# Optimization experiments

Measured on AMD Instinct MI355X. Metric: run time of the kernel, lower is better.

The kernel has to match this reference:

```python
import jax, jax.numpy as jnp
import numpy as np
from jax import lax

T_STEPS = 16
TAU = 2.0
ALPHA = 4.0  # sigmoid surrogate sharpness
BN_EPS = 1e-5


def conv1d(x, w, b, stride, pad):
    # x: [N,C,L], w: [O,I,K]
    y = lax.conv_general_dilated(x, w, (stride,), [(pad, pad)],
                                 dimension_numbers=('NCH', 'OIH', 'NCH'))
    return y + b[None, :, None]


def maxpool1d(x):  # kernel 3, stride 2, pad 1 (pad value -inf via init)
    return lax.reduce_window(x, -jnp.inf, lax.max, (1, 1, 3), (1, 1, 2),
                             [(0, 0), (0, 0), (1, 1)])


def spike(x):  # heaviside forward (surrogate only matters for bwd)
    return (x >= 0).astype(x.dtype)


def lif(x_seq):
    # multi-step LIF: v += (x - v)/tau (v_reset=0), spike at v>=1, hard reset, detach_reset
    def step(v, x):
        v = v + (x - v) / TAU
        s = spike(v - 1.0)
        v = v * (1.0 - lax.stop_gradient(s))
        return v, s
    _, s_seq = lax.scan(step, jnp.zeros_like(x_seq[0]), x_seq)
    return s_seq


def seq_apply(f, xs):
    # apply stateless layer over [T,B,...] by folding T into batch
    T, B = xs.shape[0], xs.shape[1]
    y = f(xs.reshape((T * B,) + xs.shape[2:]))
    return y.reshape((T, B) + y.shape[1:])


def setup_inputs() -> dict:
    key = jax.random.key(0)
    ks = jax.random.split(key, 12)
    B, L = 256, 4097
    inp = {
        'x': jax.random.normal(ks[0], (B, L), jnp.float32),
        'conv0_w': jax.random.normal(ks[1], (16, 1, 7), jnp.float32) * 0.2,
        'conv0_b': jax.random.normal(ks[2], (16,), jnp.float32) * 0.1,
        'bn_g': jnp.ones((16,), jnp.float32),
        'bn_b': jnp.zeros((16,), jnp.float32),
        'bn_m': jax.random.normal(ks[3], (16,), jnp.float32) * 0.1,
        'bn_v': jnp.ones((16,), jnp.float32),
        'conv1_w': jax.random.normal(ks[4], (32, 16, 5), jnp.float32) * 0.1,
        'conv1_b': jax.random.normal(ks[5], (32,), jnp.float32) * 0.1,
        'conv2_w': jax.random.normal(ks[6], (64, 32, 3), jnp.float32) * 0.1,
        'conv2_b': jax.random.normal(ks[7], (64,), jnp.float32) * 0.1,
        'fc1_w': jax.random.normal(ks[8], (32, 64), jnp.float32) * 0.12,
        'fc1_b': jax.random.normal(ks[9], (32,), jnp.float32) * 0.1,
        'fc2_w': jax.random.normal(ks[10], (5, 32), jnp.float32) * 0.17,
        'fc2_b': jax.random.normal(ks[11], (5,), jnp.float32) * 0.1,
    }
    return inp


def reference(x, conv0_w, conv0_b, bn_g, bn_b, bn_m, bn_v,
              conv1_w, conv1_b, conv2_w, conv2_b,
              fc1_w, fc1_b, fc2_w, fc2_b):
    # ---- static encoder ----
    h = x[:, None, :]                                  # [B,1,4097]
    h = conv1d(h, conv0_w, conv0_b, 2, 3)              # [B,16,2049]
    h = (h - bn_m[None, :, None]) * lax.rsqrt(bn_v + BN_EPS)[None, :, None] \
        * bn_g[None, :, None] + bn_b[None, :, None]
    h = jax.nn.relu(h)
    h = maxpool1d(h)                                   # [B,16,1025]
    # ---- repeat over T timesteps ----
    hs = jnp.broadcast_to(h[None], (T_STEPS,) + h.shape)  # [T,B,16,1025]
    # ---- spiking trunk ----
    hs = seq_apply(lambda a: conv1d(a, conv1_w, conv1_b, 2, 2), hs)  # [T,B,32,513]
    hs = lif(hs)
    hs = seq_apply(maxpool1d, hs)                      # [T,B,32,257]
    hs = seq_apply(lambda a: conv1d(a, conv2_w, conv2_b, 2, 1), hs)  # [T,B,64,129]
    hs = lif(hs)
    # dropout: identity (inference); adaptive avg pool to 1 + flatten
    hs = hs.mean(axis=-1)                              # [T,B,64]
    # ---- classifier ----
    hs = jnp.einsum('tbd,od->tbo', hs, fc1_w) + fc1_b  # [T,B,32]
    hs = lif(hs)
    hs = jnp.einsum('tbd,od->tbo', hs, fc2_w) + fc2_b  # [T,B,5]
    return hs.mean(axis=0)                             # [B,5]
```

## Files before the change

kernel.cpp:

```cpp
#include <hip/hip_runtime.h>
#include <math.h>


#define NB 256
#define LX 4097
#define LQ 2049
#define LP 1025
#define LJ1 513
#define LP1 257
#define LJ2 129

#define M1S 520
#define S2R 132
#define HSW 260

typedef float f32x4 __attribute__((ext_vector_type(4)));

__global__ __launch_bounds__(256) void kF_front(const float* __restrict__ x,
                                                const float* __restrict__ w0,
                                                const float* __restrict__ b0,
                                                const float* __restrict__ bng,
                                                const float* __restrict__ bnb,
                                                const float* __restrict__ bnm,
                                                const float* __restrict__ bnv,
                                                const float* __restrict__ w1,
                                                const float* __restrict__ b1,
                                                unsigned short* __restrict__ m1,
                                                const float* __restrict__ w2,
                                                float* __restrict__ w2t) {
  __shared__ __align__(16) float xs[1052];
  __shared__ __align__(16) float hs[16 * HSW];
  __shared__ __align__(16) float wl[2560];
  __shared__ float w0s[112];
  __shared__ float cpar[64];
  __shared__ float rs_l[16];
  int bid = blockIdx.x;
  int b = bid / 5, jt = bid % 5;
  int J0 = jt * 128;
  int Pstart = 2 * J0 - 2;
  int tid = threadIdx.x;

  if (tid < 16) rs_l[tid] = (float)(1.0 / sqrt((double)bnv[tid] + 1e-5));
  {
    const float* xb = x + (size_t)b * LX;
    int xoff = 4 * Pstart - 5;
    for (int i = tid; i < 1052; i += 256) {
      int gi = xoff + i;
      xs[i] = (gi >= 0 && gi < LX) ? xb[gi] : 0.f;
    }
    for (int i = tid; i < 2560; i += 256) {
      int c = i & 31, r = i >> 5;
      wl[i] = w1[c * 80 + r];
    }
    if (tid < 112) w0s[tid] = w0[tid];
    if (tid >= 128 && tid < 192) {
      int i = tid - 128;
      int c = i >> 2, e = i & 3;
      float v = (e == 0) ? bnm[c] : (e == 1) ? bng[c] : (e == 2) ? bnb[c] : b0[c];
      cpar[i] = v;
    }
  }
  __syncthreads();

  for (int item = tid; item < 16 * 261; item += 256) {
    int c = item / 261, dp = item - c * 261;
    int p = Pstart + dp;
    float hm = 0.f;
    if (p >= 0 && p < LP) {
      const f32x4* xv = (const f32x4*)(xs + 4 * dp);
      f32x4 a = xv[0], bq = xv[1], cq = xv[2];
      float win[12] = {a.x, a.y, a.z, a.w, bq.x, bq.y, bq.z, bq.w,
                       cq.x, cq.y, cq.z, cq.w};
      float m = cpar[4 * c], g = cpar[4 * c + 1], bb = cpar[4 * c + 2],
            bc = cpar[4 * c + 3];
      float rs = rs_l[c];
      float wv[7];
#pragma unroll
      for (int k = 0; k < 7; ++k) wv[k] = w0s[c * 7 + k];
      float best = -INFINITY;
#pragma unroll
      for (int dq = -1; dq <= 1; ++dq) {
        int q = 2 * p + dq;
        if (q < 0 || q >= LQ) continue;
        float s = 0.f;
        int base = 2 * dq + 2;
#pragma unroll
        for (int k = 0; k < 7; ++k) s = fmaf(win[base + k], wv[k], s);
        float y = s + bc;
        y = (y - m) * rs * g + bb;
        y = fmaxf(y, 0.f);
        best = fmaxf(best, y);
      }
      hm = best;
    }
    hs[c * HSW + dp] = hm;
  }
  __syncthreads();

  {
    int c = tid & 31, jg = tid >> 5;
    int jbase = J0 + jg * 16;
    if (jbase <= 512) {
      float acc[16];
#pragma unroll
      for (int i = 0; i < 16; ++i) acc[i] = 0.f;

      for (int ic = 0; ic < 16; ++ic) {
        float win[36];
        const f32x4* row = (const f32x4*)(hs + ic * HSW + 32 * jg);
#pragma unroll
        for (int i = 0; i < 9; ++i) {
          f32x4 v = row[i];
          win[4 * i] = v.x; win[4 * i + 1] = v.y;
          win[4 * i + 2] = v.z; win[4 * i + 3] = v.w;
        }
        float wv[5];
#pragma unroll
        for (int k = 0; k < 5; ++k) wv[k] = wl[(ic * 5 + k) * 32 + c];
#pragma unroll
        for (int j = 0; j < 16; ++j) {
#pragma unroll
          for (int k = 0; k < 5; ++k) acc[j] = fmaf(win[2 * j + k], wv[k], acc[j]);
        }
      }

      float bc = b1[c];
      unsigned mskv[16];
#pragma unroll
      for (int j = 0; j < 16; ++j) {
        float xin = acc[j] + bc;
        float v = 0.f; unsigned mm = 0;
#pragma unroll
        for (int t = 0; t < 16; ++t) {
          v = v + (xin - v) * 0.5f;
          if (v >= 1.f) { mm |= (1u << t); v = 0.f; }
        }
        mskv[j] = mm;
      }
      size_t rowo = ((size_t)b * 32 + c) * M1S + jbase;
      if (jbase + 15 < LJ1) {
        uint4 u0, u1;
        u0.x = mskv[0] | (mskv[1] << 16);
        u0.y = mskv[2] | (mskv[3] << 16);
        u0.z = mskv[4] | (mskv[5] << 16);
        u0.w = mskv[6] | (mskv[7] << 16);
        u1.x = mskv[8] | (mskv[9] << 16);
        u1.y = mskv[10] | (mskv[11] << 16);
        u1.z = mskv[12] | (mskv[13] << 16);
        u1.w = mskv[14] | (mskv[15] << 16);
        *(uint4*)(m1 + rowo) = u0;
        *(uint4*)(m1 + rowo + 8) = u1;
      } else {
        for (int j = 0; j < 16; ++j)
          if (jbase + j < LJ1) m1[rowo + j] = (unsigned short)mskv[j];
      }
    }
  }

  if (bid < 16) {
    for (int idx = bid * 256 + tid; idx < 64 * 32 * 3; idx += 4096) {
      int k = idx % 3; int r = idx / 3; int c = r % 32; int oc = r / 32;
      w2t[(c * 3 + k) * 64 + oc] = w2[idx];
    }
  }
}

__global__ __launch_bounds__(256) void kD_conv2_lif(const unsigned short* __restrict__ m1,
                                                    const float* __restrict__ w2t_g,
                                                    const float* __restrict__ b2,
                                                    unsigned short* __restrict__ s2) {
  __shared__ __align__(16) float F[288 * 20];
  __shared__ unsigned mval[288];
  __shared__ unsigned short mbuf[32 * 20];
  int bid = blockIdx.x;
  int b = bid / 33, jt = bid % 33;
  int j0 = jt * 4;
  int tid = threadIdx.x;
  int w = tid >> 6;
  int lane = tid & 63;

  const unsigned short* m1b = m1 + (size_t)b * 32 * M1S;
  int qbase = 4 * j0 - 3;
  for (int i = tid; i < 1024; i += 256) {
    int c = i >> 5, u = i & 31;
    if (u < 20) {
      int q = qbase + u;
      mbuf[c * 20 + u] = (q >= 0 && q <= 512) ? m1b[(size_t)c * M1S + q] : (unsigned short)0;
    }
  }
  __syncthreads();

  for (int it = tid; it < 288; it += 256) {
    int c = it / 9, idx = it - c * 9;
    int p = 2 * j0 - 1 + idx;
    unsigned m = 0;
    if (p >= 0 && p < LP1) {
      const unsigned short* mr = mbuf + c * 20;
      int l0 = 2 * idx;
      m = (unsigned)mr[l0] | (unsigned)mr[l0 + 1] | (unsigned)mr[l0 + 2];
    }
    mval[it] = m;
    f32x4* Fr = (f32x4*)(F + it * 20);
    f32x4 f0, f1, f2, f3;
    f0.x = (float)(m & 1u);         f0.y = (float)((m >> 1) & 1u);
    f0.z = (float)((m >> 2) & 1u);  f0.w = (float)((m >> 3) & 1u);
    f1.x = (float)((m >> 4) & 1u);  f1.y = (float)((m >> 5) & 1u);
    f1.z = (float)((m >> 6) & 1u);  f1.w = (float)((m >> 7) & 1u);
    f2.x = (float)((m >> 8) & 1u);  f2.y = (float)((m >> 9) & 1u);
    f2.z = (float)((m >> 10) & 1u); f2.w = (float)((m >> 11) & 1u);
    f3.x = (float)((m >> 12) & 1u); f3.y = (float)((m >> 13) & 1u);
    f3.z = (float)((m >> 14) & 1u); f3.w = (float)((m >> 15) & 1u);
    Fr[0] = f0; Fr[1] = f1; Fr[2] = f2; Fr[3] = f3;
  }
  __syncthreads();

  unsigned bits;
  {
    bool nz = false;
    if (lane < 32) {
      int base9 = lane * 9 + 2 * w;
      nz = (mval[base9] | mval[base9 + 1] | mval[base9 + 2]) != 0u;
    }
    bits = (unsigned)__ballot(nz);
  }

  float acc[16];
#pragma unroll
  for (int t = 0; t < 16; ++t) acc[t] = 0.f;

  const float* wrow = w2t_g + lane;
  while (bits) {
    int c = __builtin_ctz(bits);
    bits &= bits - 1;
    int base9 = c * 9 + 2 * w;
    unsigned mv0 = mval[base9];
    unsigned mv1 = mval[base9 + 1];
    unsigned mv2 = mval[base9 + 2];
    const float* wr = wrow + c * 192;
    const float* Fb = F + base9 * 20;
    if (mv0) {
      float wv = wr[0];
      const f32x4* Fp = (const f32x4*)Fb;
      f32x4 fv[4];
      fv[0] = Fp[0]; fv[1] = Fp[1]; fv[2] = Fp[2]; fv[3] = Fp[3];
#pragma unroll
      for (int t = 0; t < 16; ++t) acc[t] = fmaf(wv, fv[t >> 2][t & 3], acc[t]);
    }
    if (mv1) {
      float wv = wr[64];
      const f32x4* Fp = (const f32x4*)(Fb + 20);
      f32x4 fv[4];
      fv[0] = Fp[0]; fv[1] = Fp[1]; fv[2] = Fp[2]; fv[3] = Fp[3];
#pragma unroll
      for (int t = 0; t < 16; ++t) acc[t] = fmaf(wv, fv[t >> 2][t & 3], acc[t]);
    }
    if (mv2) {
      float wv = wr[128];
      const f32x4* Fp = (const f32x4*)(Fb + 40);
      f32x4 fv[4];
      fv[0] = Fp[0]; fv[1] = Fp[1]; fv[2] = Fp[2]; fv[3] = Fp[3];
#pragma unroll
      for (int t = 0; t < 16; ++t) acc[t] = fmaf(wv, fv[t >> 2][t & 3], acc[t]);
    }
  }

  int j = j0 + w;
  if (j < LJ2) {
    float bc = b2[lane];
    float v = 0.f; unsigned mm = 0;
#pragma unroll
    for (int t = 0; t < 16; ++t) {
      float xin = acc[t] + bc;
      v = v + (xin - v) * 0.5f;
      if (v >= 1.f) { mm |= (1u << t); v = 0.f; }
    }
    s2[((size_t)b * S2R + j) * 64 + lane] = (unsigned short)mm;
  }
}

__global__ __launch_bounds__(256) void kE_head(const unsigned short* __restrict__ s2,
                                               const float* __restrict__ fc1w,
                                               const float* __restrict__ fc1b,
                                               const float* __restrict__ fc2w,
                                               const float* __restrict__ fc2b,
                                               float* __restrict__ out) {
  __shared__ float meanL[16][64];
  __shared__ unsigned s3m[32];
  int b = blockIdx.x;
  int tid = threadIdx.x;
  int oc = tid >> 2, part = tid & 3;

  int jstart = (part == 0) ? 0 : 33 + (part - 1) * 32;
  int jcount = (part == 0) ? 33 : 32;
  const unsigned short* base = s2 + (size_t)b * S2R * 64 + oc;
  int cnt[16];
#pragma unroll
  for (int t = 0; t < 16; ++t) cnt[t] = 0;
  for (int u = 0; u < jcount; ++u) {
    unsigned m = base[(size_t)(jstart + u) * 64];
#pragma unroll
    for (int t = 0; t < 16; ++t) cnt[t] += (int)((m >> t) & 1u);
  }
#pragma unroll
  for (int t = 0; t < 16; ++t) {
    cnt[t] += __shfl_xor(cnt[t], 1);
    cnt[t] += __shfl_xor(cnt[t], 2);
  }
  if (part == 0) {
#pragma unroll
    for (int t = 0; t < 16; ++t) meanL[t][oc] = (float)cnt[t] / 129.f;
  }
  __syncthreads();

  if (tid < 32) {
    int o = tid;
    const float* wrow = fc1w + o * 64;
    float bb = fc1b[o];
    float v = 0.f;
    unsigned msk = 0;
    for (int t = 0; t < 16; ++t) {
      float s = 0.f;
      for (int d = 0; d < 64; ++d) s = fmaf(meanL[t][d], wrow[d], s);
      float xin = s + bb;
      v = v + (xin - v) * 0.5f;
      if (v >= 1.f) { msk |= (1u << t); v = 0.f; }
    }
    s3m[o] = msk;
  }
  __syncthreads();

  if (tid < 5) {
    int q = tid;
    const float* wrow = fc2w + q * 32;
    float bb = fc2b[q];
    float accs = 0.f;
    for (int t = 0; t < 16; ++t) {
      float s = 0.f;
      for (int o = 0; o < 32; ++o) s += (((s3m[o] >> t) & 1u) ? wrow[o] : 0.f);
      accs += (s + bb);
    }
    out[b * 5 + q] = accs / 16.f;
  }
}

extern "C" void kernel_launch(void* const* d_in, const int* in_sizes, int n_in,
                              void* d_out, int out_size, void* d_ws, size_t ws_size,
                              hipStream_t stream) {
  const float* x   = (const float*)d_in[0];
  const float* w0  = (const float*)d_in[1];
  const float* b0  = (const float*)d_in[2];
  const float* bng = (const float*)d_in[3];
  const float* bnb = (const float*)d_in[4];
  const float* bnm = (const float*)d_in[5];
  const float* bnv = (const float*)d_in[6];
  const float* w1  = (const float*)d_in[7];
  const float* b1  = (const float*)d_in[8];
  const float* w2  = (const float*)d_in[9];
  const float* b2  = (const float*)d_in[10];
  const float* f1w = (const float*)d_in[11];
  const float* f1b = (const float*)d_in[12];
  const float* f2w = (const float*)d_in[13];
  const float* f2b = (const float*)d_in[14];
  float* out = (float*)d_out;

  char* ws = (char*)d_ws;
  size_t sz_m1 = (size_t)NB * 32 * M1S * 2;
  size_t sz_s2 = (size_t)NB * S2R * 64 * 2;
  size_t off_s2 = sz_m1;
  size_t off_w2 = off_s2 + sz_s2;
  if (ws_size < off_w2 + 6144 * 4) return;

  unsigned short* m1 = (unsigned short*)ws;
  unsigned short* s2 = (unsigned short*)(ws + off_s2);
  float* w2t = (float*)(ws + off_w2);

  kF_front<<<NB * 5, 256, 0, stream>>>(x, w0, b0, bng, bnb, bnm, bnv, w1, b1, m1, w2, w2t);
  kD_conv2_lif<<<NB * 33, 256, 0, stream>>>(m1, w2t, b2, s2);
  kE_head<<<NB, 256, 0, stream>>>(s2, f1w, f1b, f2w, f2b, out);
}
```

Before: 121.1 us.

## Halve front-kernel LDS via two-pass channel staging, pack conv2 weights, rework head reduction

The front kernel now computes the pooled encoder output in two halves of 8 channels, accumulating conv1 across both passes. This halves the shared-memory staging buffer so more blocks can be resident, at the cost of extra barriers. Conv2 weights are repacked so the three taps for each (channel, out-channel) pair load as one float4 instead of three scalar loads. The head kernel now gives each wavefront a slice of positions and reduces spike counts through shared memory instead of shuffles.

```diff
diff --git a/kernel.cpp b/kernel.cpp
--- a/kernel.cpp
+++ b/kernel.cpp
@@ -27,9 +27,9 @@
                                                 const float* __restrict__ b1,
                                                 unsigned short* __restrict__ m1,
                                                 const float* __restrict__ w2,
-                                                float* __restrict__ w2t) {
+                                                float* __restrict__ w2t2) {
   __shared__ __align__(16) float xs[1052];
-  __shared__ __align__(16) float hs[16 * HSW];
+  __shared__ __align__(16) float hs[8 * HSW];
   __shared__ __align__(16) float wl[2560];
   __shared__ float w0s[112];
   __shared__ float cpar[64];
@@ -62,52 +62,62 @@
   }
   __syncthreads();
 
-  for (int item = tid; item < 16 * 261; item += 256) {
-    int c = item / 261, dp = item - c * 261;
-    int p = Pstart + dp;
-    float hm = 0.f;
-    if (p >= 0 && p < LP) {
-      const f32x4* xv = (const f32x4*)(xs + 4 * dp);
-      f32x4 a = xv[0], bq = xv[1], cq = xv[2];
-      float win[12] = {a.x, a.y, a.z, a.w, bq.x, bq.y, bq.z, bq.w,
-                       cq.x, cq.y, cq.z, cq.w};
-      float m = cpar[4 * c], g = cpar[4 * c + 1], bb = cpar[4 * c + 2],
-            bc = cpar[4 * c + 3];
-      float rs = rs_l[c];
+  int c = tid & 31, jg = tid >> 5;
+  int jbase = J0 + jg * 16;
+  bool active = (jbase <= 512);
+  float acc[16];
+#pragma unroll
+  for (int i = 0; i < 16; ++i) acc[i] = 0.f;
+
+  for (int half = 0; half < 2; ++half) {
+    {
+      int c2l = tid >> 5;
+      int g2 = tid & 31;
+      int cc = half * 8 + c2l;
+      float m = cpar[4 * cc], g = cpar[4 * cc + 1], bb = cpar[4 * cc + 2],
+            bc = cpar[4 * cc + 3];
+      float rs = rs_l[cc];
       float wv[7];
 #pragma unroll
-      for (int k = 0; k < 7; ++k) wv[k] = w0s[c * 7 + k];
-      float best = -INFINITY;
-#pragma unroll
-      for (int dq = -1; dq <= 1; ++dq) {
-        int q = 2 * p + dq;
-        if (q < 0 || q >= LQ) continue;
-        float s = 0.f;
-        int base = 2 * dq + 2;
-#pragma unroll
-        for (int k = 0; k < 7; ++k) s = fmaf(win[base + k], wv[k], s);
-        float y = s + bc;
-        y = (y - m) * rs * g + bb;
-        y = fmaxf(y, 0.f);
-        best = fmaxf(best, y);
+      for (int k = 0; k < 7; ++k) wv[k] = w0s[cc * 7 + k];
+#pragma unroll
+      for (int i = 0; i < 9; ++i) {
+        int dp = g2 * 9 + i;
+        if (dp < 261) {
+          int p = Pstart + dp;
+          float hm = 0.f;
+          if (p >= 0 && p < LP) {
+            const f32x4* xv = (const f32x4*)(xs + 4 * dp);
+            f32x4 a = xv[0], bq = xv[1], cq = xv[2];
+            float win[12] = {a.x, a.y, a.z, a.w, bq.x, bq.y, bq.z, bq.w,
+                             cq.x, cq.y, cq.z, cq.w};
+            float best = -INFINITY;
+#pragma unroll
+            for (int dq = -1; dq <= 1; ++dq) {
+              int q = 2 * p + dq;
+              if (q < 0 || q >= LQ) continue;
+              float s = 0.f;
+              int base = 2 * dq + 2;
+#pragma unroll
+              for (int k = 0; k < 7; ++k) s = fmaf(win[base + k], wv[k], s);
+              float y = s + bc;
+              y = (y - m) * rs * g + bb;
+              y = fmaxf(y, 0.f);
+              best = fmaxf(best, y);
+            }
+            hm = best;
+          }
+          hs[c2l * HSW + dp] = hm;
+        }
       }
-      hm = best;
-    }
-    hs[c * HSW + dp] = hm;
-  }
-  __syncthreads();
-
-  {
-    int c = tid & 31, jg = tid >> 5;
-    int jbase = J0 + jg * 16;
-    if (jbase <= 512) {
-      float acc[16];
-#pragma unroll
-      for (int i = 0; i < 16; ++i) acc[i] = 0.f;
-
-      for (int ic = 0; ic < 16; ++ic) {
+    }
+    __syncthreads();
+
+    if (active) {
+      for (int icl = 0; icl < 8; ++icl) {
+        int ic = half * 8 + icl;
         float win[36];
-        const f32x4* row = (const f32x4*)(hs + ic * HSW + 32 * jg);
+        const f32x4* row = (const f32x4*)(hs + icl * HSW + 32 * jg);
 #pragma unroll
         for (int i = 0; i < 9; ++i) {
           f32x4 v = row[i];
@@ -123,50 +133,53 @@
           for (int k = 0; k < 5; ++k) acc[j] = fmaf(win[2 * j + k], wv[k], acc[j]);
         }
       }
-
-      float bc = b1[c];
-      unsigned mskv[16];
-#pragma unroll
-      for (int j = 0; j < 16; ++j) {
-        float xin = acc[j] + bc;
-        float v = 0.f; unsigned mm = 0;
-#pragma unroll
-        for (int t = 0; t < 16; ++t) {
-          v = v + (xin - v) * 0.5f;
-          if (v >= 1.f) { mm |= (1u << t); v = 0.f; }
-        }
-        mskv[j] = mm;
+    }
+    __syncthreads();
+  }
+
+  if (active) {
+    float bc = b1[c];
+    unsigned mskv[16];
+#pragma unroll
+    for (int j = 0; j < 16; ++j) {
+      float xin = acc[j] + bc;
+      float v = 0.f; unsigned mm = 0;
+#pragma unroll
+      for (int t = 0; t < 16; ++t) {
+        v = v + (xin - v) * 0.5f;
+        if (v >= 1.f) { mm |= (1u << t); v = 0.f; }
       }
-      size_t rowo = ((size_t)b * 32 + c) * M1S + jbase;
-      if (jbase + 15 < LJ1) {
-        uint4 u0, u1;
-        u0.x = mskv[0] | (mskv[1] << 16);
-        u0.y = mskv[2] | (mskv[3] << 16);
-        u0.z = mskv[4] | (mskv[5] << 16);
-        u0.w = mskv[6] | (mskv[7] << 16);
-        u1.x = mskv[8] | (mskv[9] << 16);
-        u1.y = mskv[10] | (mskv[11] << 16);
-        u1.z = mskv[12] | (mskv[13] << 16);
-        u1.w = mskv[14] | (mskv[15] << 16);
-        *(uint4*)(m1 + rowo) = u0;
-        *(uint4*)(m1 + rowo + 8) = u1;
-      } else {
-        for (int j = 0; j < 16; ++j)
-          if (jbase + j < LJ1) m1[rowo + j] = (unsigned short)mskv[j];
-      }
+      mskv[j] = mm;
+    }
+    size_t rowo = ((size_t)b * 32 + c) * M1S + jbase;
+    if (jbase + 15 < LJ1) {
+      uint4 u0, u1;
+      u0.x = mskv[0] | (mskv[1] << 16);
+      u0.y = mskv[2] | (mskv[3] << 16);
+      u0.z = mskv[4] | (mskv[5] << 16);
+      u0.w = mskv[6] | (mskv[7] << 16);
+      u1.x = mskv[8] | (mskv[9] << 16);
+      u1.y = mskv[10] | (mskv[11] << 16);
+      u1.z = mskv[12] | (mskv[13] << 16);
+      u1.w = mskv[14] | (mskv[15] << 16);
+      *(uint4*)(m1 + rowo) = u0;
+      *(uint4*)(m1 + rowo + 8) = u1;
+    } else {
+      for (int j = 0; j < 16; ++j)
+        if (jbase + j < LJ1) m1[rowo + j] = (unsigned short)mskv[j];
     }
   }
 
   if (bid < 16) {
     for (int idx = bid * 256 + tid; idx < 64 * 32 * 3; idx += 4096) {
-      int k = idx % 3; int r = idx / 3; int c = r % 32; int oc = r / 32;
-      w2t[(c * 3 + k) * 64 + oc] = w2[idx];
+      int k = idx % 3; int r = idx / 3; int cc = r % 32; int oc = r / 32;
+      w2t2[((size_t)cc * 64 + oc) * 4 + k] = w2[idx];
     }
   }
 }
 
 __global__ __launch_bounds__(256) void kD_conv2_lif(const unsigned short* __restrict__ m1,
-                                                    const float* __restrict__ w2t_g,
+                                                    const float* __restrict__ w2t2,
                                                     const float* __restrict__ b2,
                                                     unsigned short* __restrict__ s2) {
   __shared__ __align__(16) float F[288 * 20];
@@ -228,7 +241,7 @@
 #pragma unroll
   for (int t = 0; t < 16; ++t) acc[t] = 0.f;
 
-  const float* wrow = w2t_g + lane;
+  const f32x4* wbase = (const f32x4*)w2t2 + lane;
   while (bits) {
     int c = __builtin_ctz(bits);
     bits &= bits - 1;
@@ -236,31 +249,28 @@
     unsigned mv0 = mval[base9];
     unsigned mv1 = mval[base9 + 1];
     unsigned mv2 = mval[base9 + 2];
-    const float* wr = wrow + c * 192;
+    f32x4 wq = wbase[c * 64];
     const float* Fb = F + base9 * 20;
     if (mv0) {
-      float wv = wr[0];
       const f32x4* Fp = (const f32x4*)Fb;
       f32x4 fv[4];
       fv[0] = Fp[0]; fv[1] = Fp[1]; fv[2] = Fp[2]; fv[3] = Fp[3];
 #pragma unroll
-      for (int t = 0; t < 16; ++t) acc[t] = fmaf(wv, fv[t >> 2][t & 3], acc[t]);
+      for (int t = 0; t < 16; ++t) acc[t] = fmaf(wq.x, fv[t >> 2][t & 3], acc[t]);
     }
     if (mv1) {
-      float wv = wr[64];
       const f32x4* Fp = (const f32x4*)(Fb + 20);
       f32x4 fv[4];
       fv[0] = Fp[0]; fv[1] = Fp[1]; fv[2] = Fp[2]; fv[3] = Fp[3];
 #pragma unroll
-      for (int t = 0; t < 16; ++t) acc[t] = fmaf(wv, fv[t >> 2][t & 3], acc[t]);
+      for (int t = 0; t < 16; ++t) acc[t] = fmaf(wq.y, fv[t >> 2][t & 3], acc[t]);
     }
     if (mv2) {
-      float wv = wr[128];
       const f32x4* Fp = (const f32x4*)(Fb + 40);
       f32x4 fv[4];
       fv[0] = Fp[0]; fv[1] = Fp[1]; fv[2] = Fp[2]; fv[3] = Fp[3];
 #pragma unroll
-      for (int t = 0; t < 16; ++t) acc[t] = fmaf(wv, fv[t >> 2][t & 3], acc[t]);
+      for (int t = 0; t < 16; ++t) acc[t] = fmaf(wq.z, fv[t >> 2][t & 3], acc[t]);
     }
   }
 
@@ -284,31 +294,34 @@
                                                const float* __restrict__ fc2w,
                                                const float* __restrict__ fc2b,
                                                float* __restrict__ out) {
+  __shared__ unsigned cntL[4][16][64];
   __shared__ float meanL[16][64];
   __shared__ unsigned s3m[32];
   int b = blockIdx.x;
   int tid = threadIdx.x;
-  int oc = tid >> 2, part = tid & 3;
-
-  int jstart = (part == 0) ? 0 : 33 + (part - 1) * 32;
-  int jcount = (part == 0) ? 33 : 32;
-  const unsigned short* base = s2 + (size_t)b * S2R * 64 + oc;
-  int cnt[16];
+  int w = tid >> 6, lane = tid & 63;
+
+  int j0 = (w == 0) ? 0 : 33 + 32 * (w - 1);
+  int jc = (w == 0) ? 33 : 32;
+  const unsigned short* base = s2 + (size_t)b * S2R * 64 + lane;
+  unsigned cnt[16];
 #pragma unroll
   for (int t = 0; t < 16; ++t) cnt[t] = 0;
-  for (int u = 0; u < jcount; ++u) {
-    unsigned m = base[(size_t)(jstart + u) * 64];
-#pragma unroll
-    for (int t = 0; t < 16; ++t) cnt[t] += (int)((m >> t) & 1u);
-  }
-#pragma unroll
-  for (int t = 0; t < 16; ++t) {
-    cnt[t] += __shfl_xor(cnt[t], 1);
-    cnt[t] += __shfl_xor(cnt[t], 2);
-  }
-  if (part == 0) {
-#pragma unroll
-    for (int t = 0; t < 16; ++t) meanL[t][oc] = (float)cnt[t] / 129.f;
+  for (int u = 0; u < jc; ++u) {
+    unsigned m = base[(size_t)(j0 + u) * 64];
+#pragma unroll
+    for (int t = 0; t < 16; ++t) cnt[t] += (m >> t) & 1u;
+  }
+#pragma unroll
+  for (int t = 0; t < 16; ++t) cntL[w][t][lane] = cnt[t];
+  __syncthreads();
+
+#pragma unroll
+  for (int i = 0; i < 4; ++i) {
+    int idx = tid + 256 * i;
+    int t = idx >> 6, oc = idx & 63;
+    unsigned s = cntL[0][t][oc] + cntL[1][t][oc] + cntL[2][t][oc] + cntL[3][t][oc];
+    meanL[t][oc] = (float)s / 129.f;
   }
   __syncthreads();
 
@@ -368,13 +381,13 @@
   size_t sz_s2 = (size_t)NB * S2R * 64 * 2;
   size_t off_s2 = sz_m1;
   size_t off_w2 = off_s2 + sz_s2;
-  if (ws_size < off_w2 + 6144 * 4) return;
+  if (ws_size < off_w2 + 32768) return;
 
   unsigned short* m1 = (unsigned short*)ws;
   unsigned short* s2 = (unsigned short*)(ws + off_s2);
-  float* w2t = (float*)(ws + off_w2);
-
-  kF_front<<<NB * 5, 256, 0, stream>>>(x, w0, b0, bng, bnb, bnm, bnv, w1, b1, m1, w2, w2t);
-  kD_conv2_lif<<<NB * 33, 256, 0, stream>>>(m1, w2t, b2, s2);
+  float* w2t2 = (float*)(ws + off_w2);
+
+  kF_front<<<NB * 5, 256, 0, stream>>>(x, w0, b0, bng, bnb, bnm, bnv, w1, b1, m1, w2, w2t2);
+  kD_conv2_lif<<<NB * 33, 256, 0, stream>>>(m1, w2t2, b2, s2);
   kE_head<<<NB, 256, 0, stream>>>(s2, f1w, f1b, f2w, f2b, out);
 }
```

Result: faster. 116.5 us (-3.8%).
